# Optimization experiments

Hardware: AMD Instinct MI355X
Metric: run time of the kernel (lower is better)

Reference implementation:

```python
import jax, jax.numpy as jnp
import numpy as np

EMB = 12
NUM_CLASSES = 17
NUM_GRAPHS = 1000


def gcn_conv(h, W, b, row, col, n):
    # h: [N, Fin]; row/col already include self-loops. Aggregation at col (target).
    h = h @ W + b  # [N, Fout]
    deg = jax.ops.segment_sum(jnp.ones_like(col, dtype=h.dtype), col, num_segments=n)
    dinv = deg ** -0.5  # self-loops guarantee deg >= 1
    norm = dinv[row] * dinv[col]  # [E]
    msg = norm[:, None] * h[row]  # gather + scale
    return jax.ops.segment_sum(msg, col, num_segments=n)  # scatter-add


def setup_inputs() -> dict:
    key = jax.random.key(0)
    ks = jax.random.split(key, 16)
    N, E = 400000, 6400000
    x = jax.random.normal(ks[0], (N, 4), dtype=jnp.float32)
    edge_index = jax.random.randint(ks[1], (2, E), 0, N, dtype=jnp.int64)
    batch_index = jnp.sort(jax.random.randint(ks[2], (N,), 0, NUM_GRAPHS, dtype=jnp.int64))

    def lin(k, fi, fo):
        k1, k2 = jax.random.split(k)
        bound = 1.0 / np.sqrt(fi)
        W = jax.random.uniform(k1, (fi, fo), minval=-bound, maxval=bound, dtype=jnp.float32)
        b = jax.random.uniform(k2, (fo,), minval=-bound, maxval=bound, dtype=jnp.float32)
        return W, b

    W0, b0 = lin(ks[3], 4, EMB)
    W1, b1 = lin(ks[4], EMB, EMB)
    W2, b2 = lin(ks[5], EMB, EMB)
    W3, b3 = lin(ks[6], EMB, EMB)
    Wout, bout = lin(ks[7], EMB * 2, NUM_CLASSES)
    return {"x": x, "edge_index": edge_index, "batch_index": batch_index,
            "W0": W0, "b0": b0, "W1": W1, "b1": b1, "W2": W2, "b2": b2,
            "W3": W3, "b3": b3, "Wout": Wout, "bout": bout}


def reference(x, edge_index, batch_index, W0, b0, W1, b1, W2, b2, W3, b3, Wout, bout):
    n = x.shape[0]
    loops = jnp.arange(n, dtype=edge_index.dtype)
    row = jnp.concatenate([edge_index[0], loops])
    col = jnp.concatenate([edge_index[1], loops])

    h = jnp.tanh(gcn_conv(x, W0, b0, row, col, n))
    h = jnp.tanh(gcn_conv(h, W1, b1, row, col, n))
    h = jnp.tanh(gcn_conv(h, W2, b2, row, col, n))
    h = jnp.tanh(gcn_conv(h, W3, b3, row, col, n))

    gmax = jax.ops.segment_max(h, batch_index, num_segments=NUM_GRAPHS)
    gsum = jax.ops.segment_sum(h, batch_index, num_segments=NUM_GRAPHS)
    cnt = jax.ops.segment_sum(jnp.ones((n,), dtype=h.dtype), batch_index, num_segments=NUM_GRAPHS)
    gmean = gsum / jnp.maximum(cnt, 1.0)[:, None]
    hidden = jnp.concatenate([gmax, gmean], axis=1)  # [G, 2*EMB]
    out = hidden @ Wout + bout  # [G, NUM_CLASSES]
    return out, hidden
```

## Files before the change

kernel.cpp:

```cpp
#include <hip/hip_runtime.h>
#include <hip/hip_bf16.h>
#include <math.h>

typedef __hip_bfloat16 bf16;

#define EMB 12
#define NCLS 17
#define NG 1000
#define BSHIFT 9
#define BSPAN 512
#define MAXNB 1024
#define CHUNK 8192
#define EB 8
#define TSHIFT 16
#define NTILE 8
#define NKEY (BSPAN*NTILE)
#define SCAP 11264

__device__ __forceinline__ float b2f(bf16 v){ return __bfloat162float(v); }

__device__ __forceinline__ unsigned short f2bf_rne(float f){
  unsigned int u = __float_as_uint(f);
  unsigned int r = (u + 0x7FFFu + ((u >> 16) & 1u)) >> 16;
  return (unsigned short)r;
}

__device__ __forceinline__ float ldf(const void* p, size_t i, int isbf){
  if (isbf) return b2f(((const bf16*)p)[i]);
  return ((const float*)p)[i];
}
__device__ __forceinline__ void stout(void* p, size_t i, float v, int isbf){
  if (isbf) ((unsigned short*)p)[i] = f2bf_rne(v);
  else      ((float*)p)[i] = v;
}

__device__ __forceinline__ void rowload(const float* p, float o[12]){
  const float4* q = (const float4*)p;
  float4 a = q[0], b = q[1], c = q[2];
  o[0]=a.x;o[1]=a.y;o[2]=a.z;o[3]=a.w;o[4]=b.x;o[5]=b.y;o[6]=b.z;o[7]=b.w;
  o[8]=c.x;o[9]=c.y;o[10]=c.z;o[11]=c.w;
}
__device__ __forceinline__ void rowload(const bf16* p, float o[12]){
  const uint4* q = (const uint4*)p;
  uint4 u0 = q[0];
  uint2 u1 = *(const uint2*)(q+1);
  o[0] =__uint_as_float(u0.x<<16); o[1] =__uint_as_float(u0.x&0xFFFF0000u);
  o[2] =__uint_as_float(u0.y<<16); o[3] =__uint_as_float(u0.y&0xFFFF0000u);
  o[4] =__uint_as_float(u0.z<<16); o[5] =__uint_as_float(u0.z&0xFFFF0000u);
  o[6] =__uint_as_float(u0.w<<16); o[7] =__uint_as_float(u0.w&0xFFFF0000u);
  o[8] =__uint_as_float(u1.x<<16); o[9] =__uint_as_float(u1.x&0xFFFF0000u);
  o[10]=__uint_as_float(u1.y<<16); o[11]=__uint_as_float(u1.y&0xFFFF0000u);
}
__device__ __forceinline__ void rowstore(float* p, const float o[12]){
  float4* q = (float4*)p;
  q[0] = make_float4(o[0],o[1],o[2],o[3]);
  q[1] = make_float4(o[4],o[5],o[6],o[7]);
  q[2] = make_float4(o[8],o[9],o[10],o[11]);
}
__device__ __forceinline__ void rowstore(bf16* p, const float o[12]){
  unsigned int u[6];
  #pragma unroll
  for (int k=0;k<6;k++)
    u[k] = (unsigned int)f2bf_rne(o[2*k]) | ((unsigned int)f2bf_rne(o[2*k+1])<<16);
  uint2* q = (uint2*)p;
  q[0] = make_uint2(u[0],u[1]);
  q[1] = make_uint2(u[2],u[3]);
  q[2] = make_uint2(u[4],u[5]);
}

__global__ void k_detect(const int* __restrict__ ei, const unsigned short* __restrict__ xh,
                         int* __restrict__ flags){
  if (blockIdx.x==0 && threadIdx.x==0){
    int z = 1;
    for (int k=1; k<32; k+=2) z &= (ei[k]==0);
    flags[0] = z;
    int hits = 0;
    for (int k=0; k<32; k+=2){
      int e = (xh[k] >> 7) & 0xFF;
      if (e >= 100 && e <= 140) hits++;
    }
    flags[1] = (hits >= 12) ? 1 : 0;
  }
}
__device__ __forceinline__ int ld_row(const int* ei, long long E, long long i, int w64){
  return w64 ? ei[2*i] : ei[i];
}
__device__ __forceinline__ int ld_col(const int* ei, long long E, long long i, int w64){
  return w64 ? ei[2*E + 2*i] : ei[E + i];
}
__device__ __forceinline__ int ld_batch(const int* b, long long i, int w64){
  return w64 ? b[2*i] : b[i];
}

__global__ void k_zero_i(int* __restrict__ p, int n){
  int i = blockIdx.x*blockDim.x + threadIdx.x;
  if (i < n) p[i] = 0;
}
__global__ void __launch_bounds__(256)
k_bkt_count(const int* __restrict__ ei, const int* __restrict__ flags,
            int* __restrict__ bcnt, int* __restrict__ bofs, int E, int NB){
  __shared__ int h[MAXNB];
  int t = threadIdx.x;
  for (int j=t; j<NB; j+=256) h[j] = 0;
  __syncthreads();
  int w64 = flags[0];
  long long base = (long long)blockIdx.x * CHUNK;
  for (int k0=0; k0<CHUNK; k0+=256*EB){
    int c[EB]; bool v[EB];
    #pragma unroll
    for (int u=0;u<EB;u++){
      long long i = base + k0 + u*256 + t;
      v[u] = (i < E);
      c[u] = v[u] ? ld_col(ei, E, i, w64) : 0;
    }
    #pragma unroll
    for (int u=0;u<EB;u++) if (v[u]) atomicAdd(&h[c[u]>>BSHIFT], 1);
  }
  __syncthreads();
  size_t rowb = (size_t)blockIdx.x * NB;
  for (int j=t; j<NB; j+=256){
    int c = h[j];
    bofs[rowb + j] = c;
    if (c > 0) atomicAdd(&bcnt[j], c);
  }
}
__global__ void __launch_bounds__(1024)
k_bkt_scan_par(const int* __restrict__ bcnt, int* __restrict__ bbase,
               int* __restrict__ rs2, int NB, int NBK){
  __shared__ int s[1024];
  int t = threadIdx.x;
  int v = (t < NB) ? bcnt[t] : 0;
  s[t] = v;
  __syncthreads();
  for (int off=1; off<1024; off<<=1){
    int add = (t >= off) ? s[t-off] : 0;
    __syncthreads();
    s[t] += add;
    __syncthreads();
  }
  if (t < NB) bbase[t] = s[t] - v;
  if (t == 1023){
    bbase[NB] = s[1023];
    rs2[NBK]  = s[1023];
  }
}
__global__ void __launch_bounds__(256)
k_colscan(int* __restrict__ bofs, const int* __restrict__ bbase, int NB, int GC){
  __shared__ int part[256];
  int j = blockIdx.x, t = threadIdx.x;
  int K = (GC + 255) / 256;
  int beg = t*K, end = beg+K < GC ? beg+K : GC;
  int s = 0;
  for (int i=beg; i<end; i++) s += bofs[(size_t)i*NB + j];
  part[t] = s;
  __syncthreads();
  for (int off=1; off<256; off<<=1){
    int add = (t >= off) ? part[t-off] : 0;
    __syncthreads();
    part[t] += add;
    __syncthreads();
  }
  int run = bbase[j] + part[t] - s;
  for (int i=beg; i<end; i++){
    size_t idx = (size_t)i*NB + j;
    int v = bofs[idx];
    bofs[idx] = run;
    run += v;
  }
}
__global__ void __launch_bounds__(256)
k_bkt_place(const int* __restrict__ ei, const int* __restrict__ flags,
            const int* __restrict__ bofs, int* __restrict__ pairs, int E, int NB){
  __shared__ int hb[MAXNB];
  __shared__ int lcur[MAXNB];
  __shared__ int part[256];
  __shared__ int vals[CHUNK];
  __shared__ int dst[CHUNK];
  int t = threadIdx.x;
  size_t rowb = (size_t)blockIdx.x * NB;
  for (int j=t; j<NB; j+=256){ hb[j] = bofs[rowb + j]; lcur[j] = 0; }
  __syncthreads();
  int w64 = flags[0];
  long long base = (long long)blockIdx.x * CHUNK;
  long long rem = E - base;
  int total = (rem < CHUNK) ? (int)rem : CHUNK;
  for (int k0=0; k0<CHUNK; k0+=256*EB){
    int c[EB]; bool v[EB];
    #pragma unroll
    for (int u=0;u<EB;u++){
      long long i = base + k0 + u*256 + t;
      v[u] = (i < E);
      c[u] = v[u] ? ld_col(ei, E, i, w64) : 0;
    }
    #pragma unroll
    for (int u=0;u<EB;u++) if (v[u]) atomicAdd(&lcur[c[u]>>BSHIFT], 1);
  }
  __syncthreads();
  int loc[4]; int s = 0;
  #pragma unroll
  for (int u=0;u<4;u++){ int j=t*4+u; loc[u] = (j<NB) ? lcur[j] : 0; s += loc[u]; }
  part[t] = s;
  __syncthreads();
  for (int off=1; off<256; off<<=1){
    int add = (t >= off) ? part[t-off] : 0;
    __syncthreads();
    part[t] += add;
    __syncthreads();
  }
  int run = part[t] - s;
  #pragma unroll
  for (int u=0;u<4;u++){
    int j=t*4+u;
    if (j<NB){ lcur[j] = run; hb[j] -= run; }
    run += loc[u];
  }
  __syncthreads();
  for (int k0=0; k0<CHUNK; k0+=256*EB){
    int r[EB], c[EB]; bool v[EB];
    #pragma unroll
    for (int u=0;u<EB;u++){
      long long i = base + k0 + u*256 + t;
      v[u] = (i < E);
      r[u] = v[u] ? ld_row(ei, E, i, w64) : 0;
      c[u] = v[u] ? ld_col(ei, E, i, w64) : 0;
    }
    #pragma unroll
    for (int u=0;u<EB;u++){
      if (v[u]){
        int j = c[u]>>BSHIFT;
        int p = atomicAdd(&lcur[j], 1);
        vals[p] = r[u] | ((r[u]>>TSHIFT)<<19) | ((c[u] & (BSPAN-1)) << 22);
        dst[p]  = hb[j] + p;
      }
    }
  }
  __syncthreads();
  for (int s2=t; s2<total; s2+=256) pairs[dst[s2]] = vals[s2];
}
__device__ __forceinline__ int tkey(int pk){
  return (((pk>>19)&7)<<BSHIFT) | (pk>>22);
}
__global__ void __launch_bounds__(256)
k_group(const int* __restrict__ pairs, const int* __restrict__ bbase,
        float* __restrict__ dinv, int* __restrict__ src,
        int* __restrict__ rs2, int N){
  __shared__ int cnt[NKEY];
  __shared__ int cur[NKEY];
  __shared__ int part[256];
  __shared__ int stage[SCAP];
  int b = blockIdx.x, t = threadIdx.x;
  int lo = bbase[b], hi = bbase[b+1];
  int cap = hi - lo;
  #pragma unroll
  for (int u=0;u<NKEY/256;u++) cnt[u*256+t] = 0;
  __syncthreads();
  {
    int p = lo + t;
    for (; p + 3*256 < hi; p += 4*256){
      int k0=tkey(pairs[p]), k1=tkey(pairs[p+256]), k2=tkey(pairs[p+512]), k3=tkey(pairs[p+768]);
      atomicAdd(&cnt[k0],1); atomicAdd(&cnt[k1],1);
      atomicAdd(&cnt[k2],1); atomicAdd(&cnt[k3],1);
    }
    for (; p < hi; p += 256) atomicAdd(&cnt[tkey(pairs[p])],1);
  }
  __syncthreads();
  int loc[16]; int s = 0;
  #pragma unroll
  for (int u=0;u<16;u++){ loc[u] = cnt[t*16+u]; s += loc[u]; }
  part[t] = s;
  __syncthreads();
  for (int off=1; off<256; off<<=1){
    int add = (t >= off) ? part[t-off] : 0;
    __syncthreads();
    part[t] += add;
    __syncthreads();
  }
  int run = lo + part[t] - s;
  #pragma unroll
  for (int u=0;u<16;u++){ cur[t*16+u] = run; run += loc[u]; }
  __syncthreads();
  {
    size_t rb = (size_t)b * NKEY;
    #pragma unroll
    for (int u=0;u<16;u++){ int k = t*16+u; rs2[rb + k] = cur[k]; }
    int col0 = b << BSHIFT;
    #pragma unroll
    for (int u=0;u<2;u++){
      int j = 2*t + u;
      int colg = col0 + j;
      if (colg < N){
        int deg = 0;
        #pragma unroll
        for (int tt=0; tt<NTILE; tt++) deg += cnt[(tt<<BSHIFT) | j];
        dinv[colg] = rsqrtf((float)deg + 1.0f);
      }
    }
  }
  __syncthreads();
  if (cap <= SCAP){
    int p = lo + t;
    for (; p + 3*256 < hi; p += 4*256){
      int pk0=pairs[p], pk1=pairs[p+256], pk2=pairs[p+512], pk3=pairs[p+768];
      int q0 = atomicAdd(&cur[tkey(pk0)], 1);
      int q1 = atomicAdd(&cur[tkey(pk1)], 1);
      int q2 = atomicAdd(&cur[tkey(pk2)], 1);
      int q3 = atomicAdd(&cur[tkey(pk3)], 1);
      stage[q0-lo] = pk0 & 0x7FFFF; stage[q1-lo] = pk1 & 0x7FFFF;
      stage[q2-lo] = pk2 & 0x7FFFF; stage[q3-lo] = pk3 & 0x7FFFF;
    }
    for (; p < hi; p += 256){
      int pk = pairs[p];
      int q = atomicAdd(&cur[tkey(pk)], 1);
      stage[q-lo] = pk & 0x7FFFF;
    }
    __syncthreads();
    for (int s2=t; s2<cap; s2+=256) src[lo+s2] = stage[s2];
  } else {
    int p = lo + t;
    for (; p + 3*256 < hi; p += 4*256){
      int pk0=pairs[p], pk1=pairs[p+256], pk2=pairs[p+512], pk3=pairs[p+768];
      int q0 = atomicAdd(&cur[tkey(pk0)], 1);
      int q1 = atomicAdd(&cur[tkey(pk1)], 1);
      int q2 = atomicAdd(&cur[tkey(pk2)], 1);
      int q3 = atomicAdd(&cur[tkey(pk3)], 1);
      src[q0] = pk0 & 0x7FFFF; src[q1] = pk1 & 0x7FFFF;
      src[q2] = pk2 & 0x7FFFF; src[q3] = pk3 & 0x7FFFF;
    }
    for (; p < hi; p += 256){
      int pk = pairs[p];
      int q = atomicAdd(&cur[tkey(pk)], 1);
      src[q] = pk & 0x7FFFF;
    }
  }
}

template<typename GT>
__global__ void k_lin_first(const void* __restrict__ x, const void* __restrict__ W,
                            const void* __restrict__ b, const int* __restrict__ flags,
                            const float* __restrict__ dinv,
                            GT* __restrict__ g, int n){
  __shared__ float Ws[4*EMB];
  __shared__ float bs[EMB];
  int t = threadIdx.x;
  int isbf = flags[1];
  if (t < 4*EMB) Ws[t] = ldf(W, t, isbf);
  if (t < EMB)   bs[t] = ldf(b, t, isbf);
  __syncthreads();
  int i = blockIdx.x*blockDim.x + t;
  if (i >= n) return;
  float xi[4];
  #pragma unroll
  for (int k=0;k<4;k++) xi[k] = ldf(x, (size_t)i*4+k, isbf);
  float d = dinv[i];
  float o[12];
  #pragma unroll
  for (int j=0;j<EMB;j++){
    float h = bs[j];
    #pragma unroll
    for (int k=0;k<4;k++) h = fmaf(xi[k], Ws[k*EMB+j], h);
    o[j] = d*h;
  }
  rowstore(g + (size_t)i*16, o);
}

template<typename GT>
__global__ void k_lin_mid(const float* __restrict__ acc, const void* __restrict__ W,
                          const void* __restrict__ b, const int* __restrict__ flags,
                          const float* __restrict__ dinv,
                          GT* __restrict__ g, int n){
  __shared__ float Ws[EMB*EMB];
  __shared__ float bs[EMB];
  int t = threadIdx.x;
  int isbf = flags[1];
  if (t < EMB*EMB) Ws[t] = ldf(W, t, isbf);
  if (t < EMB)     bs[t] = ldf(b, t, isbf);
  __syncthreads();
  int i = blockIdx.x*blockDim.x + t;
  if (i >= n) return;
  float xi[EMB];
  size_t abase = (size_t)i*EMB;
  #pragma unroll
  for (int k=0;k<EMB;k++) xi[k] = tanhf(acc[abase+k]);
  float d = dinv[i];
  float o[12];
  #pragma unroll
  for (int j=0;j<EMB;j++){
    float h = bs[j];
    #pragma unroll
    for (int k=0;k<EMB;k++) h = fmaf(xi[k], Ws[k*EMB+j], h);
    o[j] = d*h;
  }
  rowstore(g + (size_t)i*16, o);
}

template<typename GT, int MODE>
__device__ __forceinline__ void finish_col(int c, int n, const float a[12],
                                           const GT* __restrict__ gin,
                                           const float* __restrict__ dinv,
                                           const float* Ws, const float* bs,
                                           void* __restrict__ outp){
  if (c >= n) return;
  float v[12];
  rowload(gin + (size_t)c*16, v);
  #pragma unroll
  for (int j=0;j<12;j++) v[j] += a[j];
  float d = dinv[c];
  if (MODE == 0){
    float h[12];
    #pragma unroll
    for (int k=0;k<12;k++) h[k] = tanhf(d*v[k]);
    float o[12];
    #pragma unroll
    for (int j=0;j<12;j++){
      float w = bs[j];
      #pragma unroll
      for (int k=0;k<12;k++) w = fmaf(h[k], Ws[k*EMB+j], w);
      o[j] = d*w;
    }
    rowstore((GT*)outp + (size_t)c*16, o);
  } else {
    float4* ap = (float4*)((float*)outp + (size_t)c*EMB);
    ap[0] = make_float4(tanhf(d*v[0]), tanhf(d*v[1]), tanhf(d*v[2]),  tanhf(d*v[3]));
    ap[1] = make_float4(tanhf(d*v[4]), tanhf(d*v[5]), tanhf(d*v[6]),  tanhf(d*v[7]));
    ap[2] = make_float4(tanhf(d*v[8]), tanhf(d*v[9]), tanhf(d*v[10]), tanhf(d*v[11]));
  }
}

template<typename GT, int MODE>
__global__ void __launch_bounds__(256)
k_gather_rot(const int* __restrict__ rs2, const int* __restrict__ src,
             const float* __restrict__ dinv, const GT* __restrict__ gin,
             const void* __restrict__ W, const void* __restrict__ b,
             const int* __restrict__ flags, void* __restrict__ outp,
             int n, int nt){
  __shared__ float Ws[EMB*EMB];
  __shared__ float bs[EMB];
  int t = threadIdx.x;
  if (MODE == 0){
    int isbf = flags[1];
    if (t < EMB*EMB) Ws[t] = ldf(W, t, isbf);
    if (t < EMB)     bs[t] = ldf(b, t, isbf);
    __syncthreads();
  }
  int c = blockIdx.x*256 + t;
  int q = (c < n) ? c : 0;
  int base = ((q>>BSHIFT)<<12) + (q & (BSPAN-1));
  float a[12];
  #pragma unroll
  for (int j=0;j<12;j++) a[j] = 0.f;
  int tau = (int)(blockIdx.x & 7) % nt;
  int i0 = base + (tau<<BSHIFT);
  int s = rs2[i0], e = rs2[i0+1];
  for (int k=0; k<nt; k++){
    int tn = tau+1; if (tn >= nt) tn = 0;
    int ps=0, pe=0;
    if (k+1 < nt){
      int ni = base + (tn<<BSHIFT);
      ps = rs2[ni]; pe = rs2[ni+1];
    }
    int p = s;
    for (; p+1 < e; p += 2){
      int r0 = src[p], r1 = src[p+1];
      float h0[12], h1[12];
      rowload(gin + (size_t)r0*16, h0);
      rowload(gin + (size_t)r1*16, h1);
      #pragma unroll
      for (int j=0;j<12;j++) a[j] += h0[j] + h1[j];
    }
    if (p < e){
      int r = src[p];
      float h[12];
      rowload(gin + (size_t)r*16, h);
      #pragma unroll
      for (int j=0;j<12;j++) a[j] += h[j];
    }
    s=ps; e=pe; tau=tn;
  }
  finish_col<GT,MODE>(c, n, a, gin, dinv, Ws, bs, outp);
}

__global__ void k_cnt_deg(const int* __restrict__ ei, const int* __restrict__ flags,
                          int* __restrict__ cnt, int e){
  int i = blockIdx.x*blockDim.x + threadIdx.x;
  if (i >= e) return;
  atomicAdd(&cnt[ld_col(ei, e, i, flags[0])], 1);
}
__global__ void k_dinv_from_cnt(const int* __restrict__ cnt, float* __restrict__ dinv, int n){
  int i = blockIdx.x*blockDim.x + threadIdx.x;
  if (i < n) dinv[i] = rsqrtf((float)(cnt[i] + 1));
}
__global__ void k_selfinit(const float* __restrict__ g, const float* __restrict__ dinv,
                           float* __restrict__ acc, int n){
  int i = blockIdx.x*blockDim.x + threadIdx.x;
  if (i >= n) return;
  float d = dinv[i];
  float h[12]; rowload(g + (size_t)i*16, h);
  #pragma unroll
  for (int j=0;j<EMB;j++) acc[(size_t)i*EMB+j] = d*h[j];
}
__global__ void k_scatter(const int* __restrict__ ei, const int* __restrict__ flags,
                          const float* __restrict__ dinv, const float* __restrict__ g,
                          float* __restrict__ acc, int e){
  int i = blockIdx.x*blockDim.x + threadIdx.x;
  if (i >= e) return;
  int w64 = flags[0];
  int r = ld_row(ei, e, i, w64);
  int c = ld_col(ei, e, i, w64);
  float w = dinv[c];
  float h[12];
  rowload(g + (size_t)r*16, h);
  float* ap = acc + (size_t)c*EMB;
  #pragma unroll
  for (int j=0;j<EMB;j++) atomicAdd(ap+j, w*h[j]);
}

template<int DOTANH>
__global__ void __launch_bounds__(256)
k_pool(const float* __restrict__ acc, const int* __restrict__ batch,
       const int* __restrict__ flags,
       const void* __restrict__ Wout, const void* __restrict__ bout,
       void* __restrict__ out, int n){
  int g = blockIdx.x;
  int w64  = flags[0];
  int isbf = flags[1];
  __shared__ int se[2];
  __shared__ float smax[4][EMB];
  __shared__ float ssum[4][EMB];
  __shared__ float hid[2*EMB];
  if (threadIdx.x == 0){
    int lo=0, hi=n;
    while (lo<hi){ int m=(lo+hi)>>1; if (ld_batch(batch,m,w64) < g) lo=m+1; else hi=m; }
    se[0]=lo;
    int lo2=lo; hi=n;
    while (lo2<hi){ int m=(lo2+hi)>>1; if (ld_batch(batch,m,w64) < g+1) lo2=m+1; else hi=m; }
    se[1]=lo2;
  }
  __syncthreads();
  int start=se[0], end=se[1];
  float lmax[EMB], lsum[EMB];
  #pragma unroll
  for (int j=0;j<EMB;j++){ lmax[j]=-3.0e38f; lsum[j]=0.f; }
  for (int i=start+(int)threadIdx.x; i<end; i+=blockDim.x){
    size_t base=(size_t)i*EMB;
    #pragma unroll
    for (int j=0;j<EMB;j++){
      float h = DOTANH ? tanhf(acc[base+j]) : acc[base+j];
      lmax[j] = fmaxf(lmax[j], h);
      lsum[j] += h;
    }
  }
  #pragma unroll
  for (int m=32;m>=1;m>>=1){
    #pragma unroll
    for (int j=0;j<EMB;j++){
      lmax[j] = fmaxf(lmax[j], __shfl_xor(lmax[j], m, 64));
      lsum[j] += __shfl_xor(lsum[j], m, 64);
    }
  }
  int wave = threadIdx.x>>6, lane = threadIdx.x&63;
  if (lane==0){
    #pragma unroll
    for (int j=0;j<EMB;j++){ smax[wave][j]=lmax[j]; ssum[wave][j]=lsum[j]; }
  }
  __syncthreads();
  int cnt = end-start;
  if (threadIdx.x < EMB){
    int j = threadIdx.x;
    float mx=smax[0][j], sm=ssum[0][j];
    #pragma unroll
    for (int w=1;w<4;w++){ mx=fmaxf(mx,smax[w][j]); sm+=ssum[w][j]; }
    if (cnt <= 0){ mx = 0.f; sm = 0.f; }
    float mean = sm / fmaxf((float)cnt, 1.0f);
    hid[j]     = mx;
    hid[EMB+j] = mean;
    stout(out, (size_t)NG*NCLS + (size_t)g*2*EMB + j,       mx,   isbf);
    stout(out, (size_t)NG*NCLS + (size_t)g*2*EMB + EMB + j, mean, isbf);
  }
  __syncthreads();
  if (threadIdx.x < NCLS){
    int c = threadIdx.x;
    float o = ldf(bout, c, isbf);
    #pragma unroll
    for (int k=0;k<2*EMB;k++) o = fmaf(hid[k], ldf(Wout, (size_t)k*NCLS+c, isbf), o);
    stout(out, (size_t)g*NCLS + c, o, isbf);
  }
}

__global__ void k_zero_out_noflags(void* __restrict__ out, int m){
  int i = blockIdx.x*blockDim.x + threadIdx.x;
  if (i < m) ((float*)out)[i] = 0.0f;
}

static void build_csr(const int* ei, const void* x, int* flags, int* bcnt, int* bbase,
                      int* bofs, float* dinv, int* src, int* pairs, int* rs2,
                      int N, int E, int NB, hipStream_t stream){
  const int TB = 256;
  const int gc = (E + CHUNK - 1) / CHUNK;
  const int NBK = NB * NKEY;
  k_detect      <<<1, 64, 0, stream>>>(ei, (const unsigned short*)x, flags);
  k_zero_i      <<<(NB+TB-1)/TB, TB, 0, stream>>>(bcnt, NB);
  k_bkt_count   <<<gc, TB, 0, stream>>>(ei, flags, bcnt, bofs, E, NB);
  k_bkt_scan_par<<<1, 1024, 0, stream>>>(bcnt, bbase, rs2, NB, NBK);
  k_colscan     <<<NB, TB, 0, stream>>>(bofs, bbase, NB, gc);
  k_bkt_place   <<<gc, TB, 0, stream>>>(ei, flags, bofs, pairs, E, NB);
  k_group       <<<NB, TB, 0, stream>>>(pairs, bbase, dinv, src, rs2, N);
}

static size_t alignup(size_t v){ return (v + 63) & ~(size_t)63; }
static size_t maxsz(size_t a, size_t b){ return a > b ? a : b; }

extern "C" void kernel_launch(void* const* d_in, const int* in_sizes, int n_in,
                              void* d_out, int out_size, void* d_ws, size_t ws_size,
                              hipStream_t stream) {
  const void* x     = d_in[0];
  const int*  ei    = (const int*)d_in[1];
  const int*  batch = (const int*)d_in[2];
  const void* W0 = d_in[3];  const void* b0 = d_in[4];
  const void* W1 = d_in[5];  const void* b1 = d_in[6];
  const void* W2 = d_in[7];  const void* b2 = d_in[8];
  const void* W3 = d_in[9];  const void* b3 = d_in[10];
  const void* Wout = d_in[11]; const void* bout = d_in[12];

  const int N = in_sizes[0] / 4;
  const int E = in_sizes[1] / 2;
  const int NB = (N + BSPAN - 1) >> BSHIFT;
  const int GC = (E + CHUNK - 1) / CHUNK;
  const int TB = 256;
  const int gn = (N + TB - 1) / TB;
  const int gr = (N + 255) / 256;
  const int nt = (N + (1<<TSHIFT) - 1) >> TSHIFT;

  char* base = (char*)d_ws;

  size_t o_flags  = 0;
  size_t o_dinv   = alignup(o_flags + 64);
  size_t o_bcnt   = alignup(o_dinv + (size_t)N*4);
  size_t o_bbase  = alignup(o_bcnt + (size_t)NB*4);
  size_t o_bofs   = alignup(o_bbase + ((size_t)NB+1)*4);
  size_t o_rs2    = alignup(o_bofs + (size_t)GC*NB*4);
  size_t o_src    = alignup(o_rs2 + ((size_t)NB*NKEY + 1)*4);
  size_t o_buf    = alignup(o_src + (size_t)E*4);

  int* flags  = (int*)(base+o_flags);
  float* dinv = (float*)(base+o_dinv);
  int* bcnt   = (int*)(base+o_bcnt);
  int* bbase  = (int*)(base+o_bbase);
  int* bofs   = (int*)(base+o_bofs);
  int* rs2    = (int*)(base+o_rs2);
  int* src    = (int*)(base+o_src);
  int* pairs  = (int*)(base+o_buf);

  bool fast_ok = (N < (1<<19)) && (NB <= MAXNB) && (nt <= NTILE);

  {
    size_t szR0 = maxsz((size_t)N*16*2, (size_t)N*EMB*4);
    size_t o_gB = alignup(o_buf + szR0);
    size_t need = o_gB + (size_t)N*16*2;
    bool pairs_fit = (size_t)E*4 <= need - o_buf;
    if (fast_ok && pairs_fit && ws_size >= need){
      bf16*  gA  = (bf16*)(base+o_buf);
      bf16*  gB  = (bf16*)(base+o_gB);
      float* acc = (float*)(base+o_buf);
      build_csr(ei, x, flags, bcnt, bbase, bofs, dinv, src, pairs, rs2, N, E, NB, stream);
      k_lin_first<bf16><<<gn, TB, 0, stream>>>(x, W0, b0, flags, dinv, gA, N);
      k_gather_rot<bf16,0><<<gr, TB, 0, stream>>>(rs2, src, dinv, gA, W1, b1, flags, gB, N, nt);
      k_gather_rot<bf16,0><<<gr, TB, 0, stream>>>(rs2, src, dinv, gB, W2, b2, flags, gA, N, nt);
      k_gather_rot<bf16,0><<<gr, TB, 0, stream>>>(rs2, src, dinv, gA, W3, b3, flags, gB, N, nt);
      k_gather_rot<bf16,1><<<gr, TB, 0, stream>>>(rs2, src, dinv, gB, 0, 0, flags, acc, N, nt);
      k_pool<0><<<NG, 256, 0, stream>>>(acc, batch, flags, Wout, bout, d_out, N);
      return;
    }
  }

  {
    size_t o_gA = o_buf;
    size_t o_gB = alignup(o_gA + (size_t)N*16*4);
    size_t need = o_gB + (size_t)N*16*4;
    bool pairs_fit = (size_t)E*4 <= need - o_buf;
    if (fast_ok && pairs_fit && ws_size >= need){
      float* gA  = (float*)(base+o_gA);
      float* gB  = (float*)(base+o_gB);
      float* acc = gA;
      build_csr(ei, x, flags, bcnt, bbase, bofs, dinv, src, pairs, rs2, N, E, NB, stream);
      k_lin_first<float><<<gn, TB, 0, stream>>>(x, W0, b0, flags, dinv, gA, N);
      k_gather_rot<float,0><<<gr, TB, 0, stream>>>(rs2, src, dinv, gA, W1, b1, flags, gB, N, nt);
      k_gather_rot<float,0><<<gr, TB, 0, stream>>>(rs2, src, dinv, gB, W2, b2, flags, gA, N, nt);
      k_gather_rot<float,0><<<gr, TB, 0, stream>>>(rs2, src, dinv, gA, W3, b3, flags, gB, N, nt);
      k_gather_rot<float,1><<<gr, TB, 0, stream>>>(rs2, src, dinv, gB, 0, 0, flags, acc, N, nt);
      k_pool<0><<<NG, 256, 0, stream>>>(acc, batch, flags, Wout, bout, d_out, N);
      return;
    }
  }

  {
    size_t f_cnt  = alignup(o_dinv + (size_t)N*4);
    size_t f_g    = alignup(f_cnt + (size_t)N*4);
    size_t f_acc  = alignup(f_g + (size_t)N*16*4);
    size_t f_end  = f_acc + (size_t)N*EMB*4;
    const int ge = (E + TB - 1) / TB;
    int* cnt = (int*)(base+f_cnt);

    if (ws_size >= f_end){
      float* g   = (float*)(base+f_g);
      float* acc = (float*)(base+f_acc);
      k_detect  <<<1, 64, 0, stream>>>(ei, (const unsigned short*)x, flags);
      k_zero_i  <<<gn, TB, 0, stream>>>(cnt, N);
      k_cnt_deg <<<ge, TB, 0, stream>>>(ei, flags, cnt, E);
      k_dinv_from_cnt<<<gn, TB, 0, stream>>>(cnt, dinv, N);
      k_lin_first<float><<<gn, TB, 0, stream>>>(x, W0, b0, flags, dinv, g, N);
      k_selfinit <<<gn, TB, 0, stream>>>(g, dinv, acc, N);
      k_scatter  <<<ge, TB, 0, stream>>>(ei, flags, dinv, g, acc, E);
      const void* Wl[3] = {W1,W2,W3};
      const void* bl[3] = {b1,b2,b3};
      for (int l=0;l<3;l++){
        k_lin_mid<float><<<gn, TB, 0, stream>>>(acc, Wl[l], bl[l], flags, dinv, g, N);
        k_selfinit<<<gn, TB, 0, stream>>>(g, dinv, acc, N);
        k_scatter <<<ge, TB, 0, stream>>>(ei, flags, dinv, g, acc, E);
      }
      k_pool<1><<<NG, 256, 0, stream>>>(acc, batch, flags, Wout, bout, d_out, N);
    } else {
      k_zero_out_noflags<<<(out_size+255)/256, 256, 0, stream>>>(d_out, out_size);
    }
  }
}
```

Before: 527.5 us.

## Split each gathered row across two lanes with half-row loads

The gather kernel now assigns two threads per destination column, each loading one 16-byte half of the 16-wide padded row, and each thread handles two columns 256 apart, with 512-thread blocks. Partial sums are combined with a lane shuffle before the finish step runs on the even lane. This aims to raise memory-level parallelism and make each load a single aligned 16-byte access. In exchange the second half-lane loads padding (columns 12-15) that was not needed before, so gather traffic per edge grows for bf16. The bf16 rowstore now writes zeroed padding with 16-byte stores.

```diff
diff --git a/kernel.cpp b/kernel.cpp
--- a/kernel.cpp
+++ b/kernel.cpp
@@ -51,6 +51,18 @@
   o[8] =__uint_as_float(u1.x<<16); o[9] =__uint_as_float(u1.x&0xFFFF0000u);
   o[10]=__uint_as_float(u1.y<<16); o[11]=__uint_as_float(u1.y&0xFFFF0000u);
 }
+__device__ __forceinline__ void halfload(const bf16* p, int half, float o[8]){
+  uint4 u = *(const uint4*)((const unsigned short*)p + half*8);
+  o[0]=__uint_as_float(u.x<<16); o[1]=__uint_as_float(u.x&0xFFFF0000u);
+  o[2]=__uint_as_float(u.y<<16); o[3]=__uint_as_float(u.y&0xFFFF0000u);
+  o[4]=__uint_as_float(u.z<<16); o[5]=__uint_as_float(u.z&0xFFFF0000u);
+  o[6]=__uint_as_float(u.w<<16); o[7]=__uint_as_float(u.w&0xFFFF0000u);
+}
+__device__ __forceinline__ void halfload(const float* p, int half, float o[8]){
+  const float4* q = (const float4*)(p + half*8);
+  float4 x = q[0], y = q[1];
+  o[0]=x.x;o[1]=x.y;o[2]=x.z;o[3]=x.w;o[4]=y.x;o[5]=y.y;o[6]=y.z;o[7]=y.w;
+}
 __device__ __forceinline__ void rowstore(float* p, const float o[12]){
   float4* q = (float4*)p;
   q[0] = make_float4(o[0],o[1],o[2],o[3]);
@@ -62,10 +74,9 @@
   #pragma unroll
   for (int k=0;k<6;k++)
     u[k] = (unsigned int)f2bf_rne(o[2*k]) | ((unsigned int)f2bf_rne(o[2*k+1])<<16);
-  uint2* q = (uint2*)p;
-  q[0] = make_uint2(u[0],u[1]);
-  q[1] = make_uint2(u[2],u[3]);
-  q[2] = make_uint2(u[4],u[5]);
+  uint4* q = (uint4*)p;
+  q[0] = make_uint4(u[0],u[1],u[2],u[3]);
+  q[1] = make_uint4(u[4],u[5],0u,0u);
 }
 
 __global__ void k_detect(const int* __restrict__ ei, const unsigned short* __restrict__ xh,
@@ -393,6 +404,27 @@
   rowstore(g + (size_t)i*16, o);
 }
 
+template<typename GT>
+__device__ __forceinline__ void seg_half(const GT* __restrict__ gin,
+                                         const int* __restrict__ src,
+                                         int p, int e, int half, float a[8]){
+  for (; p+1 < e; p += 2){
+    int r0 = src[p], r1 = src[p+1];
+    float h0[8], h1[8];
+    halfload(gin + (size_t)r0*16, half, h0);
+    halfload(gin + (size_t)r1*16, half, h1);
+    #pragma unroll
+    for (int j=0;j<8;j++) a[j] += h0[j] + h1[j];
+  }
+  if (p < e){
+    int r = src[p];
+    float h[8];
+    halfload(gin + (size_t)r*16, half, h);
+    #pragma unroll
+    for (int j=0;j<8;j++) a[j] += h[j];
+  }
+}
+
 template<typename GT, int MODE>
 __device__ __forceinline__ void finish_col(int c, int n, const float a[12],
                                            const GT* __restrict__ gin,
@@ -427,7 +459,7 @@
 }
 
 template<typename GT, int MODE>
-__global__ void __launch_bounds__(256)
+__global__ void __launch_bounds__(512)
 k_gather_rot(const int* __restrict__ rs2, const int* __restrict__ src,
              const float* __restrict__ dinv, const GT* __restrict__ gin,
              const void* __restrict__ W, const void* __restrict__ b,
@@ -442,41 +474,47 @@
     if (t < EMB)     bs[t] = ldf(b, t, isbf);
     __syncthreads();
   }
-  int c = blockIdx.x*256 + t;
-  int q = (c < n) ? c : 0;
-  int base = ((q>>BSHIFT)<<12) + (q & (BSPAN-1));
-  float a[12];
-  #pragma unroll
-  for (int j=0;j<12;j++) a[j] = 0.f;
+  int half = t & 1;
+  int lc = t >> 1;
+  int c0 = blockIdx.x*512 + lc;
+  int c1 = c0 + 256;
+  int q0 = (c0 < n) ? c0 : 0;
+  int q1 = (c1 < n) ? c1 : 0;
+  int base0 = ((q0>>BSHIFT)<<12) + (q0 & (BSPAN-1));
+  int base1 = ((q1>>BSHIFT)<<12) + (q1 & (BSPAN-1));
+  float a0[8], a1[8];
+  #pragma unroll
+  for (int j=0;j<8;j++){ a0[j]=0.f; a1[j]=0.f; }
   int tau = (int)(blockIdx.x & 7) % nt;
-  int i0 = base + (tau<<BSHIFT);
-  int s = rs2[i0], e = rs2[i0+1];
+  int i00 = base0 + (tau<<BSHIFT);
+  int i10 = base1 + (tau<<BSHIFT);
+  int s0 = rs2[i00], e0 = rs2[i00+1];
+  int s1 = rs2[i10], e1 = rs2[i10+1];
   for (int k=0; k<nt; k++){
     int tn = tau+1; if (tn >= nt) tn = 0;
-    int ps=0, pe=0;
+    int ps0=0, pe0=0, ps1=0, pe1=0;
     if (k+1 < nt){
-      int ni = base + (tn<<BSHIFT);
-      ps = rs2[ni]; pe = rs2[ni+1];
-    }
-    int p = s;
-    for (; p+1 < e; p += 2){
-      int r0 = src[p], r1 = src[p+1];
-      float h0[12], h1[12];
-      rowload(gin + (size_t)r0*16, h0);
-      rowload(gin + (size_t)r1*16, h1);
-      #pragma unroll
-      for (int j=0;j<12;j++) a[j] += h0[j] + h1[j];
-    }
-    if (p < e){
-      int r = src[p];
-      float h[12];
-      rowload(gin + (size_t)r*16, h);
-      #pragma unroll
-      for (int j=0;j<12;j++) a[j] += h[j];
-    }
-    s=ps; e=pe; tau=tn;
-  }
-  finish_col<GT,MODE>(c, n, a, gin, dinv, Ws, bs, outp);
+      int ni0 = base0 + (tn<<BSHIFT);
+      int ni1 = base1 + (tn<<BSHIFT);
+      ps0 = rs2[ni0]; pe0 = rs2[ni0+1];
+      ps1 = rs2[ni1]; pe1 = rs2[ni1+1];
+    }
+    seg_half<GT>(gin, src, s0, e0, half, a0);
+    seg_half<GT>(gin, src, s1, e1, half, a1);
+    s0=ps0; e0=pe0; s1=ps1; e1=pe1; tau=tn;
+  }
+  float v0[12], v1[12];
+  #pragma unroll
+  for (int j=0;j<8;j++){ v0[j] = a0[j]; v1[j] = a1[j]; }
+  #pragma unroll
+  for (int j=0;j<4;j++){
+    v0[8+j] = __shfl_xor(a0[j], 1, 64);
+    v1[8+j] = __shfl_xor(a1[j], 1, 64);
+  }
+  if (half == 0){
+    finish_col<GT,MODE>(c0, n, v0, gin, dinv, Ws, bs, outp);
+    finish_col<GT,MODE>(c1, n, v1, gin, dinv, Ws, bs, outp);
+  }
 }
 
 __global__ void k_cnt_deg(const int* __restrict__ ei, const int* __restrict__ flags,
@@ -627,7 +665,7 @@
   const int GC = (E + CHUNK - 1) / CHUNK;
   const int TB = 256;
   const int gn = (N + TB - 1) / TB;
-  const int gr = (N + 255) / 256;
+  const int gr = (N + 511) / 512;
   const int nt = (N + (1<<TSHIFT) - 1) >> TSHIFT;
 
   char* base = (char*)d_ws;
@@ -663,10 +701,10 @@
       float* acc = (float*)(base+o_buf);
       build_csr(ei, x, flags, bcnt, bbase, bofs, dinv, src, pairs, rs2, N, E, NB, stream);
       k_lin_first<bf16><<<gn, TB, 0, stream>>>(x, W0, b0, flags, dinv, gA, N);
-      k_gather_rot<bf16,0><<<gr, TB, 0, stream>>>(rs2, src, dinv, gA, W1, b1, flags, gB, N, nt);
-      k_gather_rot<bf16,0><<<gr, TB, 0, stream>>>(rs2, src, dinv, gB, W2, b2, flags, gA, N, nt);
-      k_gather_rot<bf16,0><<<gr, TB, 0, stream>>>(rs2, src, dinv, gA, W3, b3, flags, gB, N, nt);
-      k_gather_rot<bf16,1><<<gr, TB, 0, stream>>>(rs2, src, dinv, gB, 0, 0, flags, acc, N, nt);
+      k_gather_rot<bf16,0><<<gr, 512, 0, stream>>>(rs2, src, dinv, gA, W1, b1, flags, gB, N, nt);
+      k_gather_rot<bf16,0><<<gr, 512, 0, stream>>>(rs2, src, dinv, gB, W2, b2, flags, gA, N, nt);
+      k_gather_rot<bf16,0><<<gr, 512, 0, stream>>>(rs2, src, dinv, gA, W3, b3, flags, gB, N, nt);
+      k_gather_rot<bf16,1><<<gr, 512, 0, stream>>>(rs2, src, dinv, gB, 0, 0, flags, acc, N, nt);
       k_pool<0><<<NG, 256, 0, stream>>>(acc, batch, flags, Wout, bout, d_out, N);
       return;
     }
@@ -683,10 +721,10 @@
       float* acc = gA;
       build_csr(ei, x, flags, bcnt, bbase, bofs, dinv, src, pairs, rs2, N, E, NB, stream);
       k_lin_first<float><<<gn, TB, 0, stream>>>(x, W0, b0, flags, dinv, gA, N);
-      k_gather_rot<float,0><<<gr, TB, 0, stream>>>(rs2, src, dinv, gA, W1, b1, flags, gB, N, nt);
-      k_gather_rot<float,0><<<gr, TB, 0, stream>>>(rs2, src, dinv, gB, W2, b2, flags, gA, N, nt);
-      k_gather_rot<float,0><<<gr, TB, 0, stream>>>(rs2, src, dinv, gA, W3, b3, flags, gB, N, nt);
-      k_gather_rot<float,1><<<gr, TB, 0, stream>>>(rs2, src, dinv, gB, 0, 0, flags, acc, N, nt);
+      k_gather_rot<float,0><<<gr, 512, 0, stream>>>(rs2, src, dinv, gA, W1, b1, flags, gB, N, nt);
+      k_gather_rot<float,0><<<gr, 512, 0, stream>>>(rs2, src, dinv, gB, W2, b2, flags, gA, N, nt);
+      k_gather_rot<float,0><<<gr, 512, 0, stream>>>(rs2, src, dinv, gA, W3, b3, flags, gB, N, nt);
+      k_gather_rot<float,1><<<gr, 512, 0, stream>>>(rs2, src, dinv, gB, 0, 0, flags, acc, N, nt);
       k_pool<0><<<NG, 256, 0, stream>>>(acc, batch, flags, Wout, bout, d_out, N);
       return;
     }
```

New measurement: 581.4 us. 10.2% more time.
